# Kernel tuning notes

Hardware: AMD Instinct MI355X
Metric: run time of the kernel (lower is better)

Reference implementation:

```python
import jax, jax.numpy as jnp
import numpy as np
from jax import lax

# Module config (mirrors init_kwargs)
N, CIN, COUT, H, W = 16, 512, 512, 64, 64
KS = 3          # conv kernel_size
FACTOR = 2
GAIN = 1.0
LRMUL = 1.0
FIR_1D = np.array([1.0, 3.0, 3.0, 1.0], dtype=np.float32)

# upfirdn pad amounts as in the torch code
FIRN = 4
P = FIRN - FACTOR + (KS - 1)      # = 4
PAD0 = (P + 1) // 2               # = 2
PAD1 = P // 2                     # = 2
W_LRMUL = GAIN / np.sqrt(CIN * COUT * KS * KS)  # he_std * lrmul (use_wscale)
B_LRMUL = LRMUL
SQRT2 = np.float32(np.sqrt(2.0))


def setup_inputs() -> dict:
    key = jax.random.key(0)
    kx, kw, kb = jax.random.split(key, 3)
    x = jax.random.normal(kx, (N, CIN, H, W), dtype=jnp.float32)
    # weight init: randn * init_std, init_std = 1/lrmul = 1.0 under use_wscale
    weight = jax.random.normal(kw, (COUT, CIN, KS, KS), dtype=jnp.float32)
    bias = jax.random.normal(kb, (COUT,), dtype=jnp.float32) * 0.1
    kf = np.outer(FIR_1D, FIR_1D)
    kf = kf / kf.sum() * GAIN
    fir = jnp.asarray(kf, dtype=jnp.float32)  # [4,4], non-trainable
    return {"x": x, "weight": weight, "bias": bias, "fir": fir}


def _blur_and_resize(x, fir):
    # x: [N, C, H, W]; FIR blur via depthwise trick: fold C into batch.
    n, c, h, w = x.shape
    y = x.reshape(n * c, 1, h, w)
    y = jnp.pad(y, ((0, 0), (0, 0), (PAD0, PAD1), (PAD0, PAD1)))
    # valid conv with 4x4 FIR -> [n*c, 1, h+1, w+1]
    y = lax.conv_general_dilated(
        y, fir[None, None, :, :], window_strides=(1, 1), padding="VALID",
        dimension_numbers=("NCHW", "OIHW", "NCHW"))
    # F.interpolate(mode='nearest') from (h+1, w+1) back to (h, w):
    # torch nearest uses src = floor(dst * in/out) == (dst*(h+1))//h
    ri = (jnp.arange(h) * (h + 1)) // h
    ci = (jnp.arange(w) * (w + 1)) // w
    y = y[:, :, ri, :][:, :, :, ci]
    return y.reshape(n, c, h, w)


def reference(x, weight, bias, fir):
    y = _blur_and_resize(x, fir)
    # strided conv: stride=factor, padding=ks//2 (SAME-ish), cross-correlation
    out = lax.conv_general_dilated(
        y, weight * W_LRMUL, window_strides=(FACTOR, FACTOR),
        padding=[(KS // 2, KS // 2), (KS // 2, KS // 2)],
        dimension_numbers=("NCHW", "OIHW", "NCHW"))
    out = out + (bias * B_LRMUL)[None, :, None, None]
    out = jnp.where(out >= 0, out, 0.2 * out) * SQRT2  # leaky_relu(0.2) * sqrt(2)
    return out
```

## Files before the change

### kernel.cpp

```cpp
#include <hip/hip_runtime.h>
#include <hip/hip_bf16.h>
#include <stdint.h>

#define N_IMG 16
#define C_IN  512
#define C_OUT 512
#define H_IN  64
#define W_IN  64
#define OH    32
#define OW    32
#define PIX   (N_IMG*OH*OW)

#define YPH 65
#define YPW 33
#define Y_SLOTS (N_IMG*YPH*2*YPW)

#define W2_ELEMS (9*C_OUT*C_IN)
#define W2_BYTES (W2_ELEMS*2)

typedef __attribute__((ext_vector_type(8))) __bf16 bf16x8;
typedef __attribute__((ext_vector_type(4))) float  f32x4;

__device__ inline void gload_lds16(const void* g, void* l) {
  __builtin_amdgcn_global_load_lds(
      (const __attribute__((address_space(1))) void*)g,
      (__attribute__((address_space(3))) void*)l, 16, 0, 0);
}

__global__ void prep_w_kernel(const float* __restrict__ w, __hip_bfloat16* __restrict__ w2) {
  int idx = blockIdx.x * 256 + threadIdx.x;
  if (idx >= W2_ELEMS) return;
  int ci  = idx & (C_IN-1);
  int rem = idx >> 9;
  int co  = rem & (C_OUT-1);
  int t   = rem >> 9;
  float v = w[((size_t)co*C_IN + ci)*9 + t] * (1.0f/1536.0f);
  w2[idx] = __float2bfloat16(v);
}

__global__ void zero_pad_kernel(__hip_bfloat16* __restrict__ yt) {
  int sid = blockIdx.x;
  size_t slot;
  if (sid < N_IMG*2*YPW) {
    int n = sid / (2*YPW);
    int v = sid % (2*YPW);
    slot = (size_t)n * (YPH*2*YPW) + v;
  } else {
    int u = sid - N_IMG*2*YPW;
    int n = u / (YPH*2);
    int v = u % (YPH*2);
    slot = ((size_t)n*(YPH*2) + v) * YPW;
  }
  ((unsigned*)yt)[slot*256 + threadIdx.x] = 0u;
}

__global__ __launch_bounds__(256) void blur_kernel(const float* __restrict__ x,
                                                   __hip_bfloat16* __restrict__ yt) {
  __shared__ float obuf[2][32][65];
  const int tid = threadIdx.x;
  const int c   = tid >> 3;
  const int p8  = tid & 7;
  const int w8  = p8 * 8;
  const int r0  = blockIdx.x * 32;
  const int cib = blockIdx.y;
  const int n   = blockIdx.z;
  const float* xc = x + ((size_t)(n*C_IN + cib*32 + c) * H_IN) * W_IN + w8;

  const int rp_oc  = tid & 3;
  const int rp_p   = tid >> 2;
  const int rp_par = rp_p & 1;
  const int rp_ch  = rp_p >> 1;

  float cur[8], nxt[8];
  float h1[8], h2[8], h3[8];
#pragma unroll
  for (int j = 0; j < 8; ++j) { h1[j] = 0.f; h2[j] = 0.f; h3[j] = 0.f; }

  auto load_row = [&](int r, float* dst) {
    if (r >= 0 && r < H_IN) {
      const float4 a = *(const float4*)(xc + (size_t)r * W_IN);
      const float4 b = *(const float4*)(xc + (size_t)r * W_IN + 4);
      dst[0]=a.x; dst[1]=a.y; dst[2]=a.z; dst[3]=a.w;
      dst[4]=b.x; dst[5]=b.y; dst[6]=b.z; dst[7]=b.w;
    } else {
#pragma unroll
      for (int j = 0; j < 8; ++j) dst[j] = 0.f;
    }
  };

  load_row(r0 - 2, cur);
  for (int ri = 0; ri < 35; ++ri) {
    const int r = r0 - 2 + ri;
    if (ri < 34) load_row(r + 1, nxt);

    float l2 = __shfl_up(cur[6], 1);
    float l1 = __shfl_up(cur[7], 1);
    float rr = __shfl_down(cur[0], 1);
    if (p8 == 0) { l2 = 0.f; l1 = 0.f; }
    if (p8 == 7) { rr = 0.f; }
    float hc[8];
    hc[0] = l2 + 3.f*(l1 + cur[0]) + cur[1];
    hc[1] = l1 + 3.f*(cur[0] + cur[1]) + cur[2];
#pragma unroll
    for (int j = 2; j < 7; ++j) hc[j] = cur[j-2] + 3.f*(cur[j-1] + cur[j]) + cur[j+1];
    hc[7] = cur[5] + 3.f*(cur[6] + cur[7]) + rr;

    if (ri >= 3) {
      const int h = r - 1;
      const int b = ri & 1;
#pragma unroll
      for (int j = 0; j < 8; ++j)
        obuf[b][c][w8 + j] = (h3[j] + 3.f*(h2[j] + h1[j]) + hc[j]) * (1.0f/64.0f);
      __syncthreads();
      alignas(16) __hip_bfloat16 t16[8];
#pragma unroll
      for (int j = 0; j < 8; ++j)
        t16[j] = __float2bfloat16(obuf[b][rp_oc*8 + j][rp_p]);
      size_t slot = ((size_t)(n*YPH + h + 1)*2 + rp_par)*YPW + rp_ch + 1;
      *(uint4*)(yt + slot*C_IN + cib*32 + rp_oc*8) = *(uint4*)t16;
    }

#pragma unroll
    for (int j = 0; j < 8; ++j) {
      h3[j] = h2[j]; h2[j] = h1[j]; h1[j] = hc[j]; cur[j] = nxt[j];
    }
  }
}

__global__ void conv_kernel(const __hip_bfloat16* __restrict__ w2,
                            const __hip_bfloat16* __restrict__ yt,
                            const float* __restrict__ bias,
                            float* __restrict__ out) {
  __shared__ __hip_bfloat16 Alds[128*64];
  __shared__ __hip_bfloat16 Blds[128*64];
  const int tid  = threadIdx.x;
  const int lane = tid & 63;
  const int wv   = tid >> 6;
  const int wm   = wv & 1;
  const int wn   = wv >> 1;
  const int cob0 = blockIdx.y * 128;
  const int pixb = blockIdx.x * 128;
  const int quad = lane >> 4;
  const int wvb  = tid & 192;

  size_t aoff[4];
  int    bseg8[4], bn65[4], boh2[4], bow_[4];
  char*  ldsAdst[4];
  char*  ldsBdst[4];
#pragma unroll
  for (int i = 0; i < 4; ++i) {
    int s = i*256 + tid;
    int r = s >> 3;
    int pp = s & 7;
    int gg = pp ^ (r & 7);
    aoff[i] = (size_t)(cob0 + r)*C_IN + gg*8;
    int gp = pixb + r;
    bn65[i] = (gp >> 10) * YPH;
    boh2[i] = ((gp >> 5) & 31) * 2;
    bow_[i] = gp & 31;
    bseg8[i] = gg*8;
    ldsAdst[i] = (char*)Alds + (size_t)(i*256 + wvb)*16;
    ldsBdst[i] = (char*)Blds + (size_t)(i*256 + wvb)*16;
  }

  f32x4 acc[4][4];
  const f32x4 zero = {0.f, 0.f, 0.f, 0.f};
#pragma unroll
  for (int mi = 0; mi < 4; ++mi)
#pragma unroll
    for (int ni = 0; ni < 4; ++ni) acc[mi][ni] = zero;

  for (int t = 0; t < 9; ++t) {
    const int kh  = t / 3;
    const int kw  = t - kh*3;
    const int par = (kw == 1) ? 0 : 1;
    const int d   = (kw == 0) ? 0 : 1;
    const __hip_bfloat16* wt = w2 + (size_t)t * C_OUT * C_IN;
    size_t boff[4];
#pragma unroll
    for (int i = 0; i < 4; ++i) {
      size_t slot = ((size_t)(bn65[i] + boh2[i] + kh)*2 + par)*YPW + bow_[i] + d;
      boff[i] = slot*C_IN + bseg8[i];
    }
    for (int cib = 0; cib < C_IN; cib += 64) {
      __syncthreads();
#pragma unroll
      for (int i = 0; i < 4; ++i) gload_lds16(wt + aoff[i] + cib, ldsAdst[i]);
#pragma unroll
      for (int i = 0; i < 4; ++i) gload_lds16(yt + boff[i] + cib, ldsBdst[i]);
      __syncthreads();
#pragma unroll
      for (int kk = 0; kk < 2; ++kk) {
        bf16x8 af[4], bfr[4];
#pragma unroll
        for (int mi = 0; mi < 4; ++mi) {
          int r = wm*64 + mi*16 + (lane & 15);
          int gsg = kk*4 + quad;
          af[mi] = *(const bf16x8*)((const char*)Alds + r*128 + ((gsg ^ (r & 7))*16));
        }
#pragma unroll
        for (int ni = 0; ni < 4; ++ni) {
          int r = wn*64 + ni*16 + (lane & 15);
          int gsg = kk*4 + quad;
          bfr[ni] = *(const bf16x8*)((const char*)Blds + r*128 + ((gsg ^ (r & 7))*16));
        }
#pragma unroll
        for (int mi = 0; mi < 4; ++mi)
#pragma unroll
          for (int ni = 0; ni < 4; ++ni)
            acc[mi][ni] = __builtin_amdgcn_mfma_f32_16x16x32_bf16(af[mi], bfr[ni], acc[mi][ni], 0, 0, 0);
      }
    }
  }

#pragma unroll
  for (int mi = 0; mi < 4; ++mi) {
#pragma unroll
    for (int reg = 0; reg < 4; ++reg) {
      int co = cob0 + wm*64 + mi*16 + quad*4 + reg;
      float bv = bias[co];
#pragma unroll
      for (int ni = 0; ni < 4; ++ni) {
        int gp  = pixb + wn*64 + ni*16 + (lane & 15);
        int n   = gp >> 10;
        int ohw = gp & 1023;
        float v = acc[mi][ni][reg] + bv;
        v = (v >= 0.f ? v : 0.2f*v) * 1.41421356f;
        out[(((size_t)n*C_OUT + co) << 10) + ohw] = v;
      }
    }
  }
}

extern "C" void kernel_launch(void* const* d_in, const int* in_sizes, int n_in,
                              void* d_out, int out_size, void* d_ws, size_t ws_size,
                              hipStream_t stream) {
  const float* x    = (const float*)d_in[0];
  const float* w    = (const float*)d_in[1];
  const float* bias = (const float*)d_in[2];
  float* out = (float*)d_out;
  __hip_bfloat16* w2 = (__hip_bfloat16*)d_ws;
  __hip_bfloat16* yt = (__hip_bfloat16*)((char*)d_ws + W2_BYTES);

  prep_w_kernel<<<(W2_ELEMS + 255)/256, 256, 0, stream>>>(w, w2);
  zero_pad_kernel<<<N_IMG*2*YPW + N_IMG*YPH*2, 256, 0, stream>>>(yt);
  blur_kernel<<<dim3(2, 16, 16), 256, 0, stream>>>(x, yt);
  conv_kernel<<<dim3(PIX/128, C_OUT/128), 256, 0, stream>>>(w2, yt, bias, out);
}
```

Before: 349.3 us.

## Double-buffer conv LDS staging, fold padding zeroing into blur, split blur rows

The conv kernel now uses two LDS buffers and a flattened 72-step loop over (tap, channel chunk). It issues the async global-to-LDS loads for the next chunk before computing the current one, with one barrier per step, so load latency overlaps MFMA work. The separate zero-padding kernel is removed and each blur block zeroes its own padding slots. The blur grid doubles with half the rows per block. The cost is twice the LDS, a launch-bounds hint, and more halo row reloads in blur.

```diff
diff --git a/kernel.cpp b/kernel.cpp
--- a/kernel.cpp
+++ b/kernel.cpp
@@ -13,7 +13,6 @@
 
 #define YPH 65
 #define YPW 33
-#define Y_SLOTS (N_IMG*YPH*2*YPW)
 
 #define W2_ELEMS (9*C_OUT*C_IN)
 #define W2_BYTES (W2_ELEMS*2)
@@ -38,22 +37,6 @@
   w2[idx] = __float2bfloat16(v);
 }
 
-__global__ void zero_pad_kernel(__hip_bfloat16* __restrict__ yt) {
-  int sid = blockIdx.x;
-  size_t slot;
-  if (sid < N_IMG*2*YPW) {
-    int n = sid / (2*YPW);
-    int v = sid % (2*YPW);
-    slot = (size_t)n * (YPH*2*YPW) + v;
-  } else {
-    int u = sid - N_IMG*2*YPW;
-    int n = u / (YPH*2);
-    int v = u % (YPH*2);
-    slot = ((size_t)n*(YPH*2) + v) * YPW;
-  }
-  ((unsigned*)yt)[slot*256 + threadIdx.x] = 0u;
-}
-
 __global__ __launch_bounds__(256) void blur_kernel(const float* __restrict__ x,
                                                    __hip_bfloat16* __restrict__ yt) {
   __shared__ float obuf[2][32][65];
@@ -61,10 +44,28 @@
   const int c   = tid >> 3;
   const int p8  = tid & 7;
   const int w8  = p8 * 8;
-  const int r0  = blockIdx.x * 32;
+  const int r0  = blockIdx.x * 16;
   const int cib = blockIdx.y;
   const int n   = blockIdx.z;
   const float* xc = x + ((size_t)(n*C_IN + cib*32 + c) * H_IN) * W_IN + w8;
+
+  {
+    const uint4 z4 = {0u, 0u, 0u, 0u};
+    if (tid < 32) {
+      int hh  = r0 + (tid >> 1);
+      int par = tid & 1;
+      size_t slot = (((size_t)n*YPH + hh + 1)*2 + par)*YPW;
+      uint4* p = (uint4*)(yt + slot*C_IN + cib*32);
+      p[0]=z4; p[1]=z4; p[2]=z4; p[3]=z4;
+    }
+    if (blockIdx.x == 0 && tid < 66) {
+      int par = tid / 33;
+      int cc  = tid - par*33;
+      size_t slot = ((size_t)n*YPH*2 + par)*YPW + cc;
+      uint4* p = (uint4*)(yt + slot*C_IN + cib*32);
+      p[0]=z4; p[1]=z4; p[2]=z4; p[3]=z4;
+    }
+  }
 
   const int rp_oc  = tid & 3;
   const int rp_p   = tid >> 2;
@@ -89,9 +90,9 @@
   };
 
   load_row(r0 - 2, cur);
-  for (int ri = 0; ri < 35; ++ri) {
+  for (int ri = 0; ri < 19; ++ri) {
     const int r = r0 - 2 + ri;
-    if (ri < 34) load_row(r + 1, nxt);
+    if (ri < 18) load_row(r + 1, nxt);
 
     float l2 = __shfl_up(cur[6], 1);
     float l1 = __shfl_up(cur[7], 1);
@@ -127,12 +128,13 @@
   }
 }
 
-__global__ void conv_kernel(const __hip_bfloat16* __restrict__ w2,
+#define ABYTES (128*64*2)
+__global__ __launch_bounds__(256, 2) void conv_kernel(const __hip_bfloat16* __restrict__ w2,
                             const __hip_bfloat16* __restrict__ yt,
                             const float* __restrict__ bias,
                             float* __restrict__ out) {
-  __shared__ __hip_bfloat16 Alds[128*64];
-  __shared__ __hip_bfloat16 Blds[128*64];
+  __shared__ __hip_bfloat16 Alds[2][128*64];
+  __shared__ __hip_bfloat16 Blds[2][128*64];
   const int tid  = threadIdx.x;
   const int lane = tid & 63;
   const int wv   = tid >> 6;
@@ -145,8 +147,7 @@
 
   size_t aoff[4];
   int    bseg8[4], bn65[4], boh2[4], bow_[4];
-  char*  ldsAdst[4];
-  char*  ldsBdst[4];
+  int    ldsOff[4];
 #pragma unroll
   for (int i = 0; i < 4; ++i) {
     int s = i*256 + tid;
@@ -159,57 +160,62 @@
     boh2[i] = ((gp >> 5) & 31) * 2;
     bow_[i] = gp & 31;
     bseg8[i] = gg*8;
-    ldsAdst[i] = (char*)Alds + (size_t)(i*256 + wvb)*16;
-    ldsBdst[i] = (char*)Blds + (size_t)(i*256 + wvb)*16;
-  }
-
-  f32x4 acc[4][4];
-  const f32x4 zero = {0.f, 0.f, 0.f, 0.f};
-#pragma unroll
-  for (int mi = 0; mi < 4; ++mi)
-#pragma unroll
-    for (int ni = 0; ni < 4; ++ni) acc[mi][ni] = zero;
-
-  for (int t = 0; t < 9; ++t) {
-    const int kh  = t / 3;
+    ldsOff[i] = (i*256 + wvb)*16;
+  }
+
+  auto stage = [&](int c, int b) {
+    const int t   = c >> 3;
+    const int cib = (c & 7) << 6;
+    const int kh  = (t * 11) >> 5;
     const int kw  = t - kh*3;
     const int par = (kw == 1) ? 0 : 1;
     const int d   = (kw == 0) ? 0 : 1;
-    const __hip_bfloat16* wt = w2 + (size_t)t * C_OUT * C_IN;
-    size_t boff[4];
+    const __hip_bfloat16* wt = w2 + (size_t)t * (C_OUT*C_IN) + cib;
+#pragma unroll
+    for (int i = 0; i < 4; ++i)
+      gload_lds16(wt + aoff[i], (char*)Alds + b*ABYTES + ldsOff[i]);
 #pragma unroll
     for (int i = 0; i < 4; ++i) {
       size_t slot = ((size_t)(bn65[i] + boh2[i] + kh)*2 + par)*YPW + bow_[i] + d;
-      boff[i] = slot*C_IN + bseg8[i];
-    }
-    for (int cib = 0; cib < C_IN; cib += 64) {
-      __syncthreads();
-#pragma unroll
-      for (int i = 0; i < 4; ++i) gload_lds16(wt + aoff[i] + cib, ldsAdst[i]);
-#pragma unroll
-      for (int i = 0; i < 4; ++i) gload_lds16(yt + boff[i] + cib, ldsBdst[i]);
-      __syncthreads();
-#pragma unroll
-      for (int kk = 0; kk < 2; ++kk) {
-        bf16x8 af[4], bfr[4];
-#pragma unroll
-        for (int mi = 0; mi < 4; ++mi) {
-          int r = wm*64 + mi*16 + (lane & 15);
-          int gsg = kk*4 + quad;
-          af[mi] = *(const bf16x8*)((const char*)Alds + r*128 + ((gsg ^ (r & 7))*16));
-        }
-#pragma unroll
-        for (int ni = 0; ni < 4; ++ni) {
-          int r = wn*64 + ni*16 + (lane & 15);
-          int gsg = kk*4 + quad;
-          bfr[ni] = *(const bf16x8*)((const char*)Blds + r*128 + ((gsg ^ (r & 7))*16));
-        }
-#pragma unroll
-        for (int mi = 0; mi < 4; ++mi)
-#pragma unroll
-          for (int ni = 0; ni < 4; ++ni)
-            acc[mi][ni] = __builtin_amdgcn_mfma_f32_16x16x32_bf16(af[mi], bfr[ni], acc[mi][ni], 0, 0, 0);
+      gload_lds16(yt + slot*C_IN + bseg8[i] + cib, (char*)Blds + b*ABYTES + ldsOff[i]);
+    }
+  };
+
+  f32x4 acc[4][4];
+  const f32x4 zero = {0.f, 0.f, 0.f, 0.f};
+#pragma unroll
+  for (int mi = 0; mi < 4; ++mi)
+#pragma unroll
+    for (int ni = 0; ni < 4; ++ni) acc[mi][ni] = zero;
+
+  stage(0, 0);
+#pragma unroll 2
+  for (int cch = 0; cch < 72; ++cch) {
+    __syncthreads();
+    if (cch < 71) stage(cch + 1, (cch + 1) & 1);
+    const int b = cch & 1;
+    const char* Ab = (const char*)Alds + b*ABYTES;
+    const char* Bb = (const char*)Blds + b*ABYTES;
+#pragma unroll
+    for (int kk = 0; kk < 2; ++kk) {
+      bf16x8 af[4], bfr[4];
+#pragma unroll
+      for (int mi = 0; mi < 4; ++mi) {
+        int r = wm*64 + mi*16 + (lane & 15);
+        int gsg = kk*4 + quad;
+        af[mi] = *(const bf16x8*)(Ab + r*128 + ((gsg ^ (r & 7))*16));
       }
+#pragma unroll
+      for (int ni = 0; ni < 4; ++ni) {
+        int r = wn*64 + ni*16 + (lane & 15);
+        int gsg = kk*4 + quad;
+        bfr[ni] = *(const bf16x8*)(Bb + r*128 + ((gsg ^ (r & 7))*16));
+      }
+#pragma unroll
+      for (int mi = 0; mi < 4; ++mi)
+#pragma unroll
+        for (int ni = 0; ni < 4; ++ni)
+          acc[mi][ni] = __builtin_amdgcn_mfma_f32_16x16x32_bf16(af[mi], bfr[ni], acc[mi][ni], 0, 0, 0);
     }
   }
 
@@ -243,7 +249,6 @@
   __hip_bfloat16* yt = (__hip_bfloat16*)((char*)d_ws + W2_BYTES);
 
   prep_w_kernel<<<(W2_ELEMS + 255)/256, 256, 0, stream>>>(w, w2);
-  zero_pad_kernel<<<N_IMG*2*YPW + N_IMG*YPH*2, 256, 0, stream>>>(yt);
-  blur_kernel<<<dim3(2, 16, 16), 256, 0, stream>>>(x, yt);
+  blur_kernel<<<dim3(4, 16, 16), 256, 0, stream>>>(x, yt);
   conv_kernel<<<dim3(PIX/128, C_OUT/128), 256, 0, stream>>>(w2, yt, bias, out);
 }
```

Result: faster. 333.7 us (-4.5%).
